# Optimization experiments

Hardware: AMD Instinct MI355X
Metric: run time of the kernel (lower is better)

The kernel has to match this reference:

```python
import jax, jax.numpy as jnp
import numpy as np

B, S, D = 64, 256, 512          # batch, seq_len_max, num_dim (= in_dim = nclass)
H, DO = 8, 64                   # num_heads, out_dim per head (H*DO == D)
ALPHA = 0.2                     # leaky_relu negative slope
N = B * S                       # nodes
DEG = 32
E = N * DEG + N                 # random edges + self-loops


def setup_inputs() -> dict:
    key = jax.random.key(0)
    k = jax.random.split(key, 7)
    h = jax.random.normal(k[0], (B, S, D), jnp.float32)
    loops = jnp.arange(N, dtype=jnp.int32)
    src = jnp.concatenate([jax.random.randint(k[1], (N * DEG,), 0, N, jnp.int32), loops])
    dst = jnp.concatenate([jax.random.randint(k[2], (N * DEG,), 0, N, jnp.int32), loops])
    W1 = jax.random.normal(k[3], (H, D, DO), jnp.float32) * 0.05      # per-head fc weight
    a1 = jax.random.normal(k[4], (H, 2 * DO), jnp.float32) * 0.05     # per-head attn_fc weight
    Wout = jax.random.normal(k[5], (H * DO, D), jnp.float32) * 0.05   # out_att fc
    aout = jax.random.normal(k[6], (2 * D,), jnp.float32) * 0.05      # out_att attn_fc
    return {"h": h, "W1": W1, "a1": a1, "Wout": Wout, "aout": aout, "src": src, "dst": dst}


def gat_head(x, W, a, src, dst, concat):
    # x: [N, in_d], W: [in_d, d], a: [2d]
    z = x @ W                                   # [N, d]
    d = W.shape[1]
    es = z @ a[:d]                              # src part of attn score, [N]
    ed = z @ a[d:]                              # dst part, [N]
    e = jax.nn.leaky_relu(es[src] + ed[dst], ALPHA)   # [E]
    # segment softmax over incoming edges of each dst node
    m = jax.ops.segment_max(e, dst, num_segments=N)
    m = jnp.where(jnp.isfinite(m), m, 0.0)
    ex = jnp.exp(e - m[dst])
    den = jax.ops.segment_sum(ex, dst, num_segments=N)
    att = ex / den[dst]                         # [E] (self-loops guarantee den > 0)
    out = jax.ops.segment_sum(att[:, None] * z[src], dst, num_segments=N)  # [N, d]
    return jax.nn.elu(out) if concat else out


def reference(h, W1, a1, Wout, aout, src, dst):
    x = h.reshape(N, D)                         # dropout is identity at eval
    heads = jax.vmap(lambda W, a: gat_head(x, W, a, src, dst, True))(W1, a1)  # [H, N, DO]
    hcat = jnp.transpose(heads, (1, 0, 2)).reshape(N, H * DO)                 # [N, H*DO]
    out = jax.nn.elu(gat_head(hcat, Wout, aout, src, dst, False))             # [N, D]
    return (out + x).reshape(B, S, D)
```

## Files before the change

### kernel.cpp

```cpp
#include <hip/hip_runtime.h>
#include <stdint.h>

#define DD 512
#define HH 8
#define DOO 64
#define ALPHA 0.2f

typedef __attribute__((ext_vector_type(8))) short short8;
typedef __attribute__((ext_vector_type(4))) float floatx4;
typedef __attribute__((ext_vector_type(4))) unsigned short u16x4;
typedef unsigned short u16;

static __device__ __forceinline__ float bf2f(u16 u){
  union { unsigned int u; float f; } c; c.u = ((unsigned int)u) << 16; return c.f;
}
static __device__ __forceinline__ u16 f2bf(float f){
  union { float f; unsigned int u; } c; c.f = f;
  unsigned int u = c.u;
  unsigned int r = (u + 0x7FFFu + ((u >> 16) & 1u)) >> 16;
  return (u16)r;
}
static __device__ __forceinline__ float leaky(float s){ return (s >= 0.f) ? s : ALPHA * s; }
static __device__ __forceinline__ float elu(float v){ return (v > 0.f) ? v : (__expf(v) - 1.f); }

#define PERM_LO 0x01000504u
#define PERM_HI 0x03020706u

#define DOT2(accv, pairv, wv) \
  asm("v_dot2_f32_bf16 %0, %1, %2, %0" : "+v"(accv) : "v"(pairv), "v"(wv))

#define GLOAD_LDS16(g, l) \
  __builtin_amdgcn_global_load_lds((const __attribute__((address_space(1))) void*)(g), \
                                   (__attribute__((address_space(3))) void*)(l), 16, 0, 0)

__global__ void k_prep(const float* __restrict__ h, u16* __restrict__ xb,
                       const float* __restrict__ W1, u16* __restrict__ wbt1,
                       const float* __restrict__ Wout, u16* __restrict__ wbt2,
                       const int* __restrict__ dst, int* deg,
                       int n4, int E){
  int i = blockIdx.x * blockDim.x + threadIdx.x;
  if (i < n4){
    float4 v = ((const float4*)h)[i];
    u16x4 o;
    o[0] = f2bf(v.x); o[1] = f2bf(v.y); o[2] = f2bf(v.z); o[3] = f2bf(v.w);
    ((u16x4*)xb)[i] = o;
    return;
  }
  i -= n4;
  if (i < HH * DD * DOO / 8){
    int idx0 = i * 8;
    #pragma unroll
    for (int t = 0; t < 8; t++){
      int idx = idx0 + t;
      int hh = idx >> 15;
      int rem = idx & 32767;
      int k = rem >> 6;
      int dd = rem & 63;
      wbt1[(hh * 64 + dd) * DD + k] = f2bf(W1[idx]);
    }
    return;
  }
  i -= HH * DD * DOO / 8;
  if (i < DD * DD){
    int k = i >> 9, n = i & 511;
    wbt2[n * DD + k] = f2bf(Wout[i]);
    return;
  }
  i -= DD * DD;
  if (i < E) atomicAdd(&deg[dst[i]], 1);
}

__global__ void k_scan(const int* __restrict__ deg, int* __restrict__ off, int N){
  __shared__ int sm[1024];
  int tid = threadIdx.x;
  const int per = 16;
  int base = tid * per;
  int loc[per];
  int t = 0;
  #pragma unroll
  for (int i = 0; i < per; i++){ int v = (base + i < N) ? deg[base + i] : 0; loc[i] = v; t += v; }
  sm[tid] = t; __syncthreads();
  for (int o = 1; o < 1024; o <<= 1){
    int v = 0;
    if (tid >= o) v = sm[tid - o];
    __syncthreads();
    sm[tid] += v;
    __syncthreads();
  }
  int run = sm[tid] - t;
  #pragma unroll
  for (int i = 0; i < per; i++){ if (base + i < N) off[base + i] = run; run += loc[i]; }
  if (tid == 1023) off[N] = run;
}

__global__ void k_scatter(const int* __restrict__ src, const int* __restrict__ dst,
                          const int* __restrict__ off, int* cursor, int* __restrict__ csr, int E){
  int i = blockIdx.x * blockDim.x + threadIdx.x;
  if (i < E){
    int d = dst[i];
    int p = atomicAdd(&cursor[d], 1);
    csr[off[d] + p] = src[i];
  }
}

__global__ __launch_bounds__(256) void k_gemm(const u16* __restrict__ A,
                                              const u16* __restrict__ BT,
                                              u16* __restrict__ C, int M){
  __shared__ __attribute__((aligned(16))) u16 As[128 * 64];
  __shared__ __attribute__((aligned(16))) u16 Bs[128 * 64];
  const int tid = threadIdx.x;
  const int wid = tid >> 6, lane = tid & 63;
  const int n0 = blockIdx.x * 128, m0 = blockIdx.y * 128;
  const int wr = wid >> 1, wc = wid & 1;
  const int row16 = lane & 15, kg = lane >> 4;
  floatx4 acc[4][4];
  #pragma unroll
  for (int i = 0; i < 4; i++)
    #pragma unroll
    for (int j = 0; j < 4; j++) acc[i][j] = (floatx4)0.0f;

  for (int kt = 0; kt < DD; kt += 64){
    #pragma unroll
    for (int i = 0; i < 4; i++){
      int chunk = i * 256 + tid;
      int m = chunk >> 3, g = chunk & 7;
      int gs = g ^ (m & 7);
      GLOAD_LDS16(A + (size_t)(m0 + m) * DD + kt + gs * 8, &As[chunk * 8]);
      GLOAD_LDS16(BT + (size_t)(n0 + m) * DD + kt + gs * 8, &Bs[chunk * 8]);
    }
    __syncthreads();
    short8 af[4][2], bf[4][2];
    #pragma unroll
    for (int mi = 0; mi < 4; mi++)
      #pragma unroll
      for (int kk = 0; kk < 2; kk++){
        int row = wr * 64 + mi * 16 + row16;
        int gr = (kk * 4 + kg) ^ (row & 7);
        af[mi][kk] = *(const short8*)(&As[(row * 8 + gr) * 8]);
      }
    #pragma unroll
    for (int ni = 0; ni < 4; ni++)
      #pragma unroll
      for (int kk = 0; kk < 2; kk++){
        int row = wc * 64 + ni * 16 + row16;
        int gr = (kk * 4 + kg) ^ (row & 7);
        bf[ni][kk] = *(const short8*)(&Bs[(row * 8 + gr) * 8]);
      }
    #pragma unroll
    for (int kk = 0; kk < 2; kk++)
      #pragma unroll
      for (int mi = 0; mi < 4; mi++)
        #pragma unroll
        for (int ni = 0; ni < 4; ni++)
          acc[mi][ni] = __builtin_amdgcn_mfma_f32_16x16x32_bf16(af[mi][kk], bf[ni][kk], acc[mi][ni], 0, 0, 0);
    __syncthreads();
  }
  #pragma unroll
  for (int mi = 0; mi < 4; mi++)
    #pragma unroll
    for (int ni = 0; ni < 4; ni++)
      #pragma unroll
      for (int j = 0; j < 4; j++){
        int r = m0 + wr * 64 + mi * 16 + kg * 4 + j;
        int c = n0 + wc * 64 + ni * 16 + row16;
        C[(size_t)r * DD + c] = f2bf(acc[mi][ni][j]);
      }
}

__global__ void k_scores1(const u16* __restrict__ z, const float* __restrict__ a1,
                          float* __restrict__ es, float* __restrict__ ed, int N){
  int wid = threadIdx.x >> 6, lane = threadIdx.x & 63;
  int n = blockIdx.x * 4 + wid;
  if (n >= N) return;
  int h = lane >> 3, j8 = lane & 7;
  short8 zv = *(const short8*)(z + (size_t)n * DD + lane * 8);
  float esv = 0.f, edv = 0.f;
  #pragma unroll
  for (int t = 0; t < 8; t++){
    float f = bf2f((u16)zv[t]);
    esv += f * a1[h * 128 + j8 * 8 + t];
    edv += f * a1[h * 128 + 64 + j8 * 8 + t];
  }
  #pragma unroll
  for (int d2 = 1; d2 < 8; d2 <<= 1){ esv += __shfl_xor(esv, d2); edv += __shfl_xor(edv, d2); }
  if (j8 == 0){ es[n * 8 + h] = esv; ed[n * 8 + h] = edv; }
}

__global__ void k_scores2(const u16* __restrict__ z, const float* __restrict__ aout,
                          float* __restrict__ es, float* __restrict__ ed, int N){
  int wid = threadIdx.x >> 6, lane = threadIdx.x & 63;
  int n = blockIdx.x * 4 + wid;
  if (n >= N) return;
  short8 zv = *(const short8*)(z + (size_t)n * DD + lane * 8);
  float esv = 0.f, edv = 0.f;
  #pragma unroll
  for (int t = 0; t < 8; t++){
    float f = bf2f((u16)zv[t]);
    esv += f * aout[lane * 8 + t];
    edv += f * aout[512 + lane * 8 + t];
  }
  #pragma unroll
  for (int d2 = 1; d2 < 64; d2 <<= 1){ esv += __shfl_xor(esv, d2); edv += __shfl_xor(edv, d2); }
  if (lane == 0){ es[n] = esv; ed[n] = edv; }
}

__global__ __launch_bounds__(256) void k_agg1(const u16* __restrict__ z,
    const float* __restrict__ es, const float* __restrict__ ed,
    const int* __restrict__ off, const int* __restrict__ csr,
    u16* __restrict__ hcat, int N){
  int wid = threadIdx.x >> 6, lane = threadIdx.x & 63;
  int n = blockIdx.x * 4 + wid;
  if (n >= N) return;
  int p = blockIdx.y;
  int o0 = off[n], cnt = off[n + 1] - o0;
  int g = lane >> 4, li = lane & 15;
  int myhead = 2 * p + (lane >> 5);
  int hoff = (li >> 3) << 5;
  int coloff = p * 128 + li * 8;
  const u16* zc = z + coloff;
  float edn = ed[(size_t)n * 8 + myhead];
  float acc[8];
  #pragma unroll
  for (int j = 0; j < 8; j++) acc[j] = 0.f;
  float den = 0.f;
  int el = lane & 31;

  for (int base = 0; base < cnt; base += 32){
    int e = base + el;
    int sv = 0; float av = 0.f;
    if (e < cnt){
      sv = csr[o0 + e];
      av = __expf(leaky(es[(size_t)sv * 8 + myhead] + edn));
      den += av;
    }
    float av1 = __shfl_xor(av, 1);
    unsigned apk;
    asm("v_cvt_pk_bf16_f32 %0, %1, %2" : "=v"(apk) : "v"(av), "v"(av1));
    int m = cnt - base; if (m > 32) m = 32;
    int itn = (m + 7) >> 3;
    for (int it = 0; it < itn; it++){
      int q = it * 4 + g;
      int sb0 = __shfl(sv, 2 * q);
      int sb1 = __shfl(sv, 2 * q + 1);
      unsigned aq = __shfl(apk, hoff + 2 * q);
      uint4 z0 = *(const uint4*)(zc + (size_t)sb0 * DD);
      uint4 z1 = *(const uint4*)(zc + (size_t)sb1 * DD);
      unsigned pr;
      pr = __builtin_amdgcn_perm(z0.x, z1.x, PERM_LO); DOT2(acc[0], pr, aq);
      pr = __builtin_amdgcn_perm(z0.x, z1.x, PERM_HI); DOT2(acc[1], pr, aq);
      pr = __builtin_amdgcn_perm(z0.y, z1.y, PERM_LO); DOT2(acc[2], pr, aq);
      pr = __builtin_amdgcn_perm(z0.y, z1.y, PERM_HI); DOT2(acc[3], pr, aq);
      pr = __builtin_amdgcn_perm(z0.z, z1.z, PERM_LO); DOT2(acc[4], pr, aq);
      pr = __builtin_amdgcn_perm(z0.z, z1.z, PERM_HI); DOT2(acc[5], pr, aq);
      pr = __builtin_amdgcn_perm(z0.w, z1.w, PERM_LO); DOT2(acc[6], pr, aq);
      pr = __builtin_amdgcn_perm(z0.w, z1.w, PERM_HI); DOT2(acc[7], pr, aq);
    }
  }
  #pragma unroll
  for (int d2 = 1; d2 < 32; d2 <<= 1) den += __shfl_xor(den, d2);
  #pragma unroll
  for (int j = 0; j < 8; j++){
    acc[j] += __shfl_xor(acc[j], 16);
    acc[j] += __shfl_xor(acc[j], 32);
  }
  float dh = __shfl(den, hoff);
  if (lane < 16){
    float inv = 1.f / dh;
    short8 o;
    #pragma unroll
    for (int j = 0; j < 8; j++) o[j] = (short)f2bf(elu(acc[j] * inv));
    *(short8*)(hcat + (size_t)n * DD + coloff) = o;
  }
}

__global__ __launch_bounds__(256) void k_agg2(const u16* __restrict__ z,
    const float* __restrict__ es, const float* __restrict__ ed,
    const int* __restrict__ off, const int* __restrict__ csr,
    const u16* __restrict__ xb, float* __restrict__ out, int N){
  int wid = threadIdx.x >> 6, lane = threadIdx.x & 63;
  int n = blockIdx.x * 4 + wid;
  if (n >= N) return;
  int p = blockIdx.y;
  int o0 = off[n], cnt = off[n + 1] - o0;
  int g = lane >> 4, li = lane & 15;
  int coloff = p * 128 + li * 8;
  const u16* zc = z + coloff;
  float edn = ed[n];
  float acc[8];
  #pragma unroll
  for (int j = 0; j < 8; j++) acc[j] = 0.f;
  float den = 0.f;
  int el = lane & 31;

  for (int base = 0; base < cnt; base += 32){
    int e = base + el;
    int sv = 0; float av = 0.f;
    if (e < cnt){
      sv = csr[o0 + e];
      av = __expf(leaky(es[sv] + edn));
      if (lane < 32) den += av;
    }
    float av1 = __shfl_xor(av, 1);
    unsigned apk;
    asm("v_cvt_pk_bf16_f32 %0, %1, %2" : "=v"(apk) : "v"(av), "v"(av1));
    int m = cnt - base; if (m > 32) m = 32;
    int itn = (m + 7) >> 3;
    for (int it = 0; it < itn; it++){
      int q = it * 4 + g;
      int sb0 = __shfl(sv, 2 * q);
      int sb1 = __shfl(sv, 2 * q + 1);
      unsigned aq = __shfl(apk, 2 * q);
      uint4 z0 = *(const uint4*)(zc + (size_t)sb0 * DD);
      uint4 z1 = *(const uint4*)(zc + (size_t)sb1 * DD);
      unsigned pr;
      pr = __builtin_amdgcn_perm(z0.x, z1.x, PERM_LO); DOT2(acc[0], pr, aq);
      pr = __builtin_amdgcn_perm(z0.x, z1.x, PERM_HI); DOT2(acc[1], pr, aq);
      pr = __builtin_amdgcn_perm(z0.y, z1.y, PERM_LO); DOT2(acc[2], pr, aq);
      pr = __builtin_amdgcn_perm(z0.y, z1.y, PERM_HI); DOT2(acc[3], pr, aq);
      pr = __builtin_amdgcn_perm(z0.z, z1.z, PERM_LO); DOT2(acc[4], pr, aq);
      pr = __builtin_amdgcn_perm(z0.z, z1.z, PERM_HI); DOT2(acc[5], pr, aq);
      pr = __builtin_amdgcn_perm(z0.w, z1.w, PERM_LO); DOT2(acc[6], pr, aq);
      pr = __builtin_amdgcn_perm(z0.w, z1.w, PERM_HI); DOT2(acc[7], pr, aq);
    }
  }
  #pragma unroll
  for (int d2 = 1; d2 < 64; d2 <<= 1) den += __shfl_xor(den, d2);
  #pragma unroll
  for (int j = 0; j < 8; j++){
    acc[j] += __shfl_xor(acc[j], 16);
    acc[j] += __shfl_xor(acc[j], 32);
  }
  if (lane < 16){
    float inv = 1.f / den;
    short8 xv = *(const short8*)(xb + (size_t)n * DD + coloff);
    float ov[8];
    #pragma unroll
    for (int j = 0; j < 8; j++) ov[j] = elu(acc[j] * inv) + bf2f((u16)xv[j]);
    float4 o0v, o1v;
    o0v.x = ov[0]; o0v.y = ov[1]; o0v.z = ov[2]; o0v.w = ov[3];
    o1v.x = ov[4]; o1v.y = ov[5]; o1v.z = ov[6]; o1v.w = ov[7];
    *(float4*)(out + (size_t)n * DD + coloff) = o0v;
    *(float4*)(out + (size_t)n * DD + coloff + 4) = o1v;
  }
}

extern "C" void kernel_launch(void* const* d_in, const int* in_sizes, int n_in,
                              void* d_out, int out_size, void* d_ws, size_t ws_size,
                              hipStream_t stream){
  const float* h   = (const float*)d_in[0];
  const float* W1  = (const float*)d_in[1];
  const float* a1  = (const float*)d_in[2];
  const float* Wout= (const float*)d_in[3];
  const float* aout= (const float*)d_in[4];
  const int* src   = (const int*)d_in[5];
  const int* dst   = (const int*)d_in[6];
  float* out = (float*)d_out;
  const int N = in_sizes[0] / DD;
  const int E = in_sizes[5];

  char* p = (char*)d_ws;
  auto alloc = [&](size_t bytes) -> char* {
    char* r = p;
    p += (bytes + 255) & ~(size_t)255;
    return r;
  };
  u16* xb    = (u16*)alloc((size_t)N * DD * 2);
  u16* z1b   = (u16*)alloc((size_t)N * DD * 2);
  u16* hcat  = (u16*)alloc((size_t)N * DD * 2);
  u16* wbt1  = (u16*)alloc((size_t)DD * DD * 2);
  u16* wbt2  = (u16*)alloc((size_t)DD * DD * 2);
  float* es1 = (float*)alloc((size_t)N * HH * 4);
  float* ed1 = (float*)alloc((size_t)N * HH * 4);
  float* es2 = (float*)alloc((size_t)N * 4);
  float* ed2 = (float*)alloc((size_t)N * 4);
  int* deg   = (int*)alloc((size_t)N * 4);
  int* off   = (int*)alloc((size_t)(N + 1) * 4);
  int* cursor= (int*)alloc((size_t)N * 4);
  int* csr   = (int*)alloc((size_t)E * 4);

  hipMemsetAsync(deg, 0, (size_t)((char*)csr - (char*)deg), stream);

  int n4 = N * DD / 4;
  int prep_threads = n4 + HH * DD * DOO / 8 + DD * DD + E;
  k_prep<<<(prep_threads + 255) / 256, 256, 0, stream>>>(h, xb, W1, wbt1, Wout, wbt2, dst, deg, n4, E);
  k_scan<<<1, 1024, 0, stream>>>(deg, off, N);
  k_scatter<<<(E + 255) / 256, 256, 0, stream>>>(src, dst, off, cursor, csr, E);

  dim3 gg(DD / 128, N / 128);
  dim3 ga((N + 3) / 4, 4);
  k_gemm<<<gg, 256, 0, stream>>>(xb, wbt1, z1b, N);
  k_scores1<<<(N + 3) / 4, 256, 0, stream>>>(z1b, a1, es1, ed1, N);
  k_agg1<<<ga, 256, 0, stream>>>(z1b, es1, ed1, off, csr, hcat, N);

  k_gemm<<<gg, 256, 0, stream>>>(hcat, wbt2, z1b, N);
  k_scores2<<<(N + 3) / 4, 256, 0, stream>>>(z1b, aout, es2, ed2, N);
  k_agg2<<<ga, 256, 0, stream>>>(z1b, es2, ed2, off, csr, xb, out, N);
}
```

Measured before the change: 234.8 us.

## Precompute packed edge weights and software-pipeline gather loops in aggregation

Pads each node's CSR segment to an even length and adds per-graph-layer edge-weight kernels that compute exp(leaky) attention weights once per edge and head. The weights are stored as packed bf16 pairs, along with per-node softmax denominators. The aggregation kernels then read int2 source pairs and packed weights directly, with no redundant exp/shuffle work across the four column-group blocks. They also double-buffer the z gathers so loads for the next pairs are in flight while the current dot products run. The cost is two extra launches and extra workspace traffic for the weight arrays, plus padding entries that contribute zero-weight gathers of node 0.

```diff
diff --git a/kernel.cpp b/kernel.cpp
--- a/kernel.cpp
+++ b/kernel.cpp
@@ -28,6 +28,17 @@
 
 #define DOT2(accv, pairv, wv) \
   asm("v_dot2_f32_bf16 %0, %1, %2, %0" : "+v"(accv) : "v"(pairv), "v"(wv))
+
+#define DOTS8(ZA, ZB, AQ) do{ unsigned pr_; \
+  pr_=__builtin_amdgcn_perm((ZA).x,(ZB).x,PERM_LO); DOT2(acc[0],pr_,(AQ)); \
+  pr_=__builtin_amdgcn_perm((ZA).x,(ZB).x,PERM_HI); DOT2(acc[1],pr_,(AQ)); \
+  pr_=__builtin_amdgcn_perm((ZA).y,(ZB).y,PERM_LO); DOT2(acc[2],pr_,(AQ)); \
+  pr_=__builtin_amdgcn_perm((ZA).y,(ZB).y,PERM_HI); DOT2(acc[3],pr_,(AQ)); \
+  pr_=__builtin_amdgcn_perm((ZA).z,(ZB).z,PERM_LO); DOT2(acc[4],pr_,(AQ)); \
+  pr_=__builtin_amdgcn_perm((ZA).z,(ZB).z,PERM_HI); DOT2(acc[5],pr_,(AQ)); \
+  pr_=__builtin_amdgcn_perm((ZA).w,(ZB).w,PERM_LO); DOT2(acc[6],pr_,(AQ)); \
+  pr_=__builtin_amdgcn_perm((ZA).w,(ZB).w,PERM_HI); DOT2(acc[7],pr_,(AQ)); \
+}while(0)
 
 #define GLOAD_LDS16(g, l) \
   __builtin_amdgcn_global_load_lds((const __attribute__((address_space(1))) void*)(g), \
@@ -78,7 +89,11 @@
   int loc[per];
   int t = 0;
   #pragma unroll
-  for (int i = 0; i < per; i++){ int v = (base + i < N) ? deg[base + i] : 0; loc[i] = v; t += v; }
+  for (int i = 0; i < per; i++){
+    int v = (base + i < N) ? deg[base + i] : 0;
+    v = (v + 1) & ~1;
+    loc[i] = v; t += v;
+  }
   sm[tid] = t; __syncthreads();
   for (int o = 1; o < 1024; o <<= 1){
     int v = 0;
@@ -204,68 +219,159 @@
   if (lane == 0){ es[n] = esv; ed[n] = edv; }
 }
 
+__global__ void k_edgew1(const float* __restrict__ es, const float* __restrict__ ed,
+                         const int* __restrict__ off, const int* __restrict__ deg,
+                         int* __restrict__ csr, unsigned* __restrict__ wp,
+                         float* __restrict__ den1, int N, int ep2){
+  int wid = threadIdx.x >> 6, lane = threadIdx.x & 63;
+  int n = blockIdx.x * 4 + wid;
+  if (n >= N) return;
+  int o0 = off[n], cntp = off[n + 1] - o0, cnt = deg[n];
+  float edh[8];
+  {
+    float4 d0 = *(const float4*)(ed + (size_t)n * 8);
+    float4 d1 = *(const float4*)(ed + (size_t)n * 8 + 4);
+    edh[0]=d0.x; edh[1]=d0.y; edh[2]=d0.z; edh[3]=d0.w;
+    edh[4]=d1.x; edh[5]=d1.y; edh[6]=d1.z; edh[7]=d1.w;
+  }
+  float den[8];
+  #pragma unroll
+  for (int h = 0; h < 8; h++) den[h] = 0.f;
+  for (int base = 0; base < cntp; base += 64){
+    int e = base + lane;
+    float wv[8];
+    if (e < cnt){
+      int s = csr[o0 + e];
+      float4 e0 = *(const float4*)(es + (size_t)s * 8);
+      float4 e1 = *(const float4*)(es + (size_t)s * 8 + 4);
+      float ev[8] = {e0.x, e0.y, e0.z, e0.w, e1.x, e1.y, e1.z, e1.w};
+      #pragma unroll
+      for (int h = 0; h < 8; h++){
+        float w = __expf(leaky(ev[h] + edh[h]));
+        wv[h] = w; den[h] += w;
+      }
+    } else {
+      if (e < cntp) csr[o0 + e] = 0;
+      #pragma unroll
+      for (int h = 0; h < 8; h++) wv[h] = 0.f;
+    }
+    #pragma unroll
+    for (int h = 0; h < 8; h++){
+      float wn = __shfl_down(wv[h], 1);
+      if (!(lane & 1) && e < cntp){
+        unsigned pk;
+        asm("v_cvt_pk_bf16_f32 %0, %1, %2" : "=v"(pk) : "v"(wv[h]), "v"(wn));
+        wp[(size_t)h * ep2 + ((o0 + e) >> 1)] = pk;
+      }
+    }
+  }
+  #pragma unroll
+  for (int h = 0; h < 8; h++){
+    float d = den[h];
+    #pragma unroll
+    for (int d2 = 1; d2 < 64; d2 <<= 1) d += __shfl_xor(d, d2);
+    if (lane == 0) den1[(size_t)n * 8 + h] = d;
+  }
+}
+
+__global__ void k_edgew2(const float* __restrict__ es, const float* __restrict__ ed,
+                         const int* __restrict__ off, const int* __restrict__ deg,
+                         int* __restrict__ csr, unsigned* __restrict__ wp,
+                         float* __restrict__ den2, int N){
+  int wid = threadIdx.x >> 6, lane = threadIdx.x & 63;
+  int n = blockIdx.x * 4 + wid;
+  if (n >= N) return;
+  int o0 = off[n], cntp = off[n + 1] - o0, cnt = deg[n];
+  float edn = ed[n];
+  float dsum = 0.f;
+  for (int base = 0; base < cntp; base += 64){
+    int e = base + lane;
+    float w = 0.f;
+    if (e < cnt){
+      int s = csr[o0 + e];
+      w = __expf(leaky(es[s] + edn));
+      dsum += w;
+    } else if (e < cntp){
+      csr[o0 + e] = 0;
+    }
+    float wn = __shfl_down(w, 1);
+    if (!(lane & 1) && e < cntp){
+      unsigned pk;
+      asm("v_cvt_pk_bf16_f32 %0, %1, %2" : "=v"(pk) : "v"(w), "v"(wn));
+      wp[(o0 + e) >> 1] = pk;
+    }
+  }
+  #pragma unroll
+  for (int d2 = 1; d2 < 64; d2 <<= 1) dsum += __shfl_xor(dsum, d2);
+  if (lane == 0) den2[n] = dsum;
+}
+
 __global__ __launch_bounds__(256) void k_agg1(const u16* __restrict__ z,
-    const float* __restrict__ es, const float* __restrict__ ed,
+    const unsigned* __restrict__ wp, const float* __restrict__ den1,
     const int* __restrict__ off, const int* __restrict__ csr,
-    u16* __restrict__ hcat, int N){
+    u16* __restrict__ hcat, int N, int ep2){
   int wid = threadIdx.x >> 6, lane = threadIdx.x & 63;
   int n = blockIdx.x * 4 + wid;
   if (n >= N) return;
   int p = blockIdx.y;
-  int o0 = off[n], cnt = off[n + 1] - o0;
+  int o0 = off[n];
+  int npairs = (off[n + 1] - o0) >> 1;
+  int qb = o0 >> 1;
   int g = lane >> 4, li = lane & 15;
-  int myhead = 2 * p + (lane >> 5);
-  int hoff = (li >> 3) << 5;
+  int head = 2 * p + (li >> 3);
+  const unsigned* wph = wp + (size_t)head * ep2 + qb;
+  const int2* cp = (const int2*)csr + qb;
   int coloff = p * 128 + li * 8;
   const u16* zc = z + coloff;
-  float edn = ed[(size_t)n * 8 + myhead];
   float acc[8];
   #pragma unroll
   for (int j = 0; j < 8; j++) acc[j] = 0.f;
-  float den = 0.f;
-  int el = lane & 31;
-
-  for (int base = 0; base < cnt; base += 32){
-    int e = base + el;
-    int sv = 0; float av = 0.f;
-    if (e < cnt){
-      sv = csr[o0 + e];
-      av = __expf(leaky(es[(size_t)sv * 8 + myhead] + edn));
-      den += av;
-    }
-    float av1 = __shfl_xor(av, 1);
-    unsigned apk;
-    asm("v_cvt_pk_bf16_f32 %0, %1, %2" : "=v"(apk) : "v"(av), "v"(av1));
-    int m = cnt - base; if (m > 32) m = 32;
-    int itn = (m + 7) >> 3;
-    for (int it = 0; it < itn; it++){
-      int q = it * 4 + g;
-      int sb0 = __shfl(sv, 2 * q);
-      int sb1 = __shfl(sv, 2 * q + 1);
-      unsigned aq = __shfl(apk, hoff + 2 * q);
-      uint4 z0 = *(const uint4*)(zc + (size_t)sb0 * DD);
-      uint4 z1 = *(const uint4*)(zc + (size_t)sb1 * DD);
-      unsigned pr;
-      pr = __builtin_amdgcn_perm(z0.x, z1.x, PERM_LO); DOT2(acc[0], pr, aq);
-      pr = __builtin_amdgcn_perm(z0.x, z1.x, PERM_HI); DOT2(acc[1], pr, aq);
-      pr = __builtin_amdgcn_perm(z0.y, z1.y, PERM_LO); DOT2(acc[2], pr, aq);
-      pr = __builtin_amdgcn_perm(z0.y, z1.y, PERM_HI); DOT2(acc[3], pr, aq);
-      pr = __builtin_amdgcn_perm(z0.z, z1.z, PERM_LO); DOT2(acc[4], pr, aq);
-      pr = __builtin_amdgcn_perm(z0.z, z1.z, PERM_HI); DOT2(acc[5], pr, aq);
-      pr = __builtin_amdgcn_perm(z0.w, z1.w, PERM_LO); DOT2(acc[6], pr, aq);
-      pr = __builtin_amdgcn_perm(z0.w, z1.w, PERM_HI); DOT2(acc[7], pr, aq);
-    }
-  }
-  #pragma unroll
-  for (int d2 = 1; d2 < 32; d2 <<= 1) den += __shfl_xor(den, d2);
+
+  uint4 zA0 = {0,0,0,0}, zA1 = {0,0,0,0}, zB0 = {0,0,0,0}, zB1 = {0,0,0,0};
+  unsigned aqA = 0, aqB = 0;
+  {
+    int q0 = g, q1 = 4 + g;
+    if (q0 < npairs){
+      int2 sp = cp[q0]; aqA = wph[q0];
+      zA0 = *(const uint4*)(zc + (size_t)sp.x * DD);
+      zA1 = *(const uint4*)(zc + (size_t)sp.y * DD);
+    }
+    if (q1 < npairs){
+      int2 sp = cp[q1]; aqB = wph[q1];
+      zB0 = *(const uint4*)(zc + (size_t)sp.x * DD);
+      zB1 = *(const uint4*)(zc + (size_t)sp.y * DD);
+    }
+  }
+  int itn = (npairs + 3) >> 2;
+  for (int it = 2; it < itn + 2; it += 2){
+    int q2 = it * 4 + g, q3 = q2 + 4;
+    bool v2 = q2 < npairs, v3 = q3 < npairs;
+    int2 sp2 = {0,0}, sp3 = {0,0};
+    unsigned naqA = 0, naqB = 0;
+    if (v2){ sp2 = cp[q2]; naqA = wph[q2]; }
+    if (v3){ sp3 = cp[q3]; naqB = wph[q3]; }
+    DOTS8(zA0, zA1, aqA);
+    uint4 nzA0 = {0,0,0,0}, nzA1 = {0,0,0,0};
+    if (v2){
+      nzA0 = *(const uint4*)(zc + (size_t)sp2.x * DD);
+      nzA1 = *(const uint4*)(zc + (size_t)sp2.y * DD);
+    }
+    DOTS8(zB0, zB1, aqB);
+    uint4 nzB0 = {0,0,0,0}, nzB1 = {0,0,0,0};
+    if (v3){
+      nzB0 = *(const uint4*)(zc + (size_t)sp3.x * DD);
+      nzB1 = *(const uint4*)(zc + (size_t)sp3.y * DD);
+    }
+    zA0 = nzA0; zA1 = nzA1; aqA = naqA;
+    zB0 = nzB0; zB1 = nzB1; aqB = naqB;
+  }
   #pragma unroll
   for (int j = 0; j < 8; j++){
     acc[j] += __shfl_xor(acc[j], 16);
     acc[j] += __shfl_xor(acc[j], 32);
   }
-  float dh = __shfl(den, hoff);
   if (lane < 16){
-    float inv = 1.f / dh;
+    float inv = 1.f / den1[(size_t)n * 8 + head];
     short8 o;
     #pragma unroll
     for (int j = 0; j < 8; j++) o[j] = (short)f2bf(elu(acc[j] * inv));
@@ -274,64 +380,70 @@
 }
 
 __global__ __launch_bounds__(256) void k_agg2(const u16* __restrict__ z,
-    const float* __restrict__ es, const float* __restrict__ ed,
+    const unsigned* __restrict__ wp, const float* __restrict__ den2,
     const int* __restrict__ off, const int* __restrict__ csr,
     const u16* __restrict__ xb, float* __restrict__ out, int N){
   int wid = threadIdx.x >> 6, lane = threadIdx.x & 63;
   int n = blockIdx.x * 4 + wid;
   if (n >= N) return;
   int p = blockIdx.y;
-  int o0 = off[n], cnt = off[n + 1] - o0;
+  int o0 = off[n];
+  int npairs = (off[n + 1] - o0) >> 1;
+  int qb = o0 >> 1;
   int g = lane >> 4, li = lane & 15;
+  const unsigned* wph = wp + qb;
+  const int2* cp = (const int2*)csr + qb;
   int coloff = p * 128 + li * 8;
   const u16* zc = z + coloff;
-  float edn = ed[n];
   float acc[8];
   #pragma unroll
   for (int j = 0; j < 8; j++) acc[j] = 0.f;
-  float den = 0.f;
-  int el = lane & 31;
-
-  for (int base = 0; base < cnt; base += 32){
-    int e = base + el;
-    int sv = 0; float av = 0.f;
-    if (e < cnt){
-      sv = csr[o0 + e];
-      av = __expf(leaky(es[sv] + edn));
-      if (lane < 32) den += av;
-    }
-    float av1 = __shfl_xor(av, 1);
-    unsigned apk;
-    asm("v_cvt_pk_bf16_f32 %0, %1, %2" : "=v"(apk) : "v"(av), "v"(av1));
-    int m = cnt - base; if (m > 32) m = 32;
-    int itn = (m + 7) >> 3;
-    for (int it = 0; it < itn; it++){
-      int q = it * 4 + g;
-      int sb0 = __shfl(sv, 2 * q);
-      int sb1 = __shfl(sv, 2 * q + 1);
-      unsigned aq = __shfl(apk, 2 * q);
-      uint4 z0 = *(const uint4*)(zc + (size_t)sb0 * DD);
-      uint4 z1 = *(const uint4*)(zc + (size_t)sb1 * DD);
-      unsigned pr;
-      pr = __builtin_amdgcn_perm(z0.x, z1.x, PERM_LO); DOT2(acc[0], pr, aq);
-      pr = __builtin_amdgcn_perm(z0.x, z1.x, PERM_HI); DOT2(acc[1], pr, aq);
-      pr = __builtin_amdgcn_perm(z0.y, z1.y, PERM_LO); DOT2(acc[2], pr, aq);
-      pr = __builtin_amdgcn_perm(z0.y, z1.y, PERM_HI); DOT2(acc[3], pr, aq);
-      pr = __builtin_amdgcn_perm(z0.z, z1.z, PERM_LO); DOT2(acc[4], pr, aq);
-      pr = __builtin_amdgcn_perm(z0.z, z1.z, PERM_HI); DOT2(acc[5], pr, aq);
-      pr = __builtin_amdgcn_perm(z0.w, z1.w, PERM_LO); DOT2(acc[6], pr, aq);
-      pr = __builtin_amdgcn_perm(z0.w, z1.w, PERM_HI); DOT2(acc[7], pr, aq);
-    }
-  }
-  #pragma unroll
-  for (int d2 = 1; d2 < 64; d2 <<= 1) den += __shfl_xor(den, d2);
+
+  uint4 zA0 = {0,0,0,0}, zA1 = {0,0,0,0}, zB0 = {0,0,0,0}, zB1 = {0,0,0,0};
+  unsigned aqA = 0, aqB = 0;
+  {
+    int q0 = g, q1 = 4 + g;
+    if (q0 < npairs){
+      int2 sp = cp[q0]; aqA = wph[q0];
+      zA0 = *(const uint4*)(zc + (size_t)sp.x * DD);
+      zA1 = *(const uint4*)(zc + (size_t)sp.y * DD);
+    }
+    if (q1 < npairs){
+      int2 sp = cp[q1]; aqB = wph[q1];
+      zB0 = *(const uint4*)(zc + (size_t)sp.x * DD);
+      zB1 = *(const uint4*)(zc + (size_t)sp.y * DD);
+    }
+  }
+  int itn = (npairs + 3) >> 2;
+  for (int it = 2; it < itn + 2; it += 2){
+    int q2 = it * 4 + g, q3 = q2 + 4;
+    bool v2 = q2 < npairs, v3 = q3 < npairs;
+    int2 sp2 = {0,0}, sp3 = {0,0};
+    unsigned naqA = 0, naqB = 0;
+    if (v2){ sp2 = cp[q2]; naqA = wph[q2]; }
+    if (v3){ sp3 = cp[q3]; naqB = wph[q3]; }
+    DOTS8(zA0, zA1, aqA);
+    uint4 nzA0 = {0,0,0,0}, nzA1 = {0,0,0,0};
+    if (v2){
+      nzA0 = *(const uint4*)(zc + (size_t)sp2.x * DD);
+      nzA1 = *(const uint4*)(zc + (size_t)sp2.y * DD);
+    }
+    DOTS8(zB0, zB1, aqB);
+    uint4 nzB0 = {0,0,0,0}, nzB1 = {0,0,0,0};
+    if (v3){
+      nzB0 = *(const uint4*)(zc + (size_t)sp3.x * DD);
+      nzB1 = *(const uint4*)(zc + (size_t)sp3.y * DD);
+    }
+    zA0 = nzA0; zA1 = nzA1; aqA = naqA;
+    zB0 = nzB0; zB1 = nzB1; aqB = naqB;
+  }
   #pragma unroll
   for (int j = 0; j < 8; j++){
     acc[j] += __shfl_xor(acc[j], 16);
     acc[j] += __shfl_xor(acc[j], 32);
   }
   if (lane < 16){
-    float inv = 1.f / den;
+    float inv = 1.f / den2[n];
     short8 xv = *(const short8*)(xb + (size_t)n * DD + coloff);
     float ov[8];
     #pragma unroll
@@ -357,6 +469,8 @@
   float* out = (float*)d_out;
   const int N = in_sizes[0] / DD;
   const int E = in_sizes[5];
+  const int EP = E + N;
+  const int ep2 = EP >> 1;
 
   char* p = (char*)d_ws;
   auto alloc = [&](size_t bytes) -> char* {
@@ -373,10 +487,14 @@
   float* ed1 = (float*)alloc((size_t)N * HH * 4);
   float* es2 = (float*)alloc((size_t)N * 4);
   float* ed2 = (float*)alloc((size_t)N * 4);
+  float* den1= (float*)alloc((size_t)N * HH * 4);
+  float* den2= (float*)alloc((size_t)N * 4);
   int* deg   = (int*)alloc((size_t)N * 4);
   int* off   = (int*)alloc((size_t)(N + 1) * 4);
   int* cursor= (int*)alloc((size_t)N * 4);
-  int* csr   = (int*)alloc((size_t)E * 4);
+  int* csr   = (int*)alloc((size_t)EP * 4);
+  unsigned* wp1 = (unsigned*)alloc((size_t)HH * ep2 * 4);
+  unsigned* wp2 = (unsigned*)alloc((size_t)ep2 * 4);
 
   hipMemsetAsync(deg, 0, (size_t)((char*)csr - (char*)deg), stream);
 
@@ -388,11 +506,15 @@
 
   dim3 gg(DD / 128, N / 128);
   dim3 ga((N + 3) / 4, 4);
+  dim3 gw((N + 3) / 4);
+
   k_gemm<<<gg, 256, 0, stream>>>(xb, wbt1, z1b, N);
   k_scores1<<<(N + 3) / 4, 256, 0, stream>>>(z1b, a1, es1, ed1, N);
-  k_agg1<<<ga, 256, 0, stream>>>(z1b, es1, ed1, off, csr, hcat, N);
+  k_edgew1<<<gw, 256, 0, stream>>>(es1, ed1, off, deg, csr, wp1, den1, N, ep2);
+  k_agg1<<<ga, 256, 0, stream>>>(z1b, wp1, den1, off, csr, hcat, N, ep2);
 
   k_gemm<<<gg, 256, 0, stream>>>(hcat, wbt2, z1b, N);
   k_scores2<<<(N + 3) / 4, 256, 0, stream>>>(z1b, aout, es2, ed2, N);
-  k_agg2<<<ga, 256, 0, stream>>>(z1b, es2, ed2, off, csr, xb, out, N);
-}
+  k_edgew2<<<gw, 256, 0, stream>>>(es2, ed2, off, deg, csr, wp2, den2, N);
+  k_agg2<<<ga, 256, 0, stream>>>(z1b, wp2, den2, off, csr, xb, out, N);
+}
```

New measurement: 250.0 us. +6.5%, slower.
